# Optimization experiments

Measured on AMD Instinct MI355X. Metric: run time of the kernel, lower is better.

The kernel has to match this reference:

```python
import jax, jax.numpy as jnp
import numpy as np

N = 100000          # nodes
E = 1600000         # directed edges (before self-loops)
F_IN = 500          # num_features
HID = 16            # hidden_dim
HEADS = 8
NUM_CLASSES = 10
NEG_SLOPE = 0.2     # PyG GATConv default
BN_EPS = 1e-5


def setup_inputs() -> dict:
    key = jax.random.key(0)
    ks = jax.random.split(key, 20)
    def glorot(k, shape):
        fan = shape[0] + shape[-1]
        return jax.random.normal(k, shape, jnp.float32) * jnp.sqrt(2.0 / fan)
    x = jax.random.normal(ks[0], (N, F_IN), jnp.float32)
    edge_index = jax.random.randint(ks[1], (2, E), 0, N, dtype=jnp.int32)
    inp = {
        'x': x, 'edge_index': edge_index,
        # conv1: F_IN -> HID, 8 heads
        'W1': glorot(ks[2], (F_IN, HEADS * HID)),
        'a1_src': glorot(ks[3], (HEADS, HID)),
        'a1_dst': glorot(ks[4], (HEADS, HID)),
        'b1': jnp.zeros((HEADS * HID,), jnp.float32),
        'g1': jnp.ones((HEADS * HID,), jnp.float32),
        'be1': jnp.zeros((HEADS * HID,), jnp.float32),
        # conv2: 128 -> HID, 8 heads
        'W2': glorot(ks[5], (HEADS * HID, HEADS * HID)),
        'a2_src': glorot(ks[6], (HEADS, HID)),
        'a2_dst': glorot(ks[7], (HEADS, HID)),
        'b2': jnp.zeros((HEADS * HID,), jnp.float32),
        'g2': jnp.ones((HEADS * HID,), jnp.float32),
        'be2': jnp.zeros((HEADS * HID,), jnp.float32),
        # conv3: 128 -> NUM_CLASSES, 1 head
        'W3': glorot(ks[8], (HEADS * HID, NUM_CLASSES)),
        'a3_src': glorot(ks[9], (1, NUM_CLASSES)),
        'a3_dst': glorot(ks[10], (1, NUM_CLASSES)),
        'b3': jnp.zeros((NUM_CLASSES,), jnp.float32),
    }
    return inp


def gat_conv(x, src, dst, W, a_src, a_dst, b, heads, out_ch):
    n = x.shape[0]
    h = (x @ W).reshape(n, heads, out_ch)                      # [N,H,C]
    al_src = jnp.einsum('nhc,hc->nh', h, a_src)                # [N,H]
    al_dst = jnp.einsum('nhc,hc->nh', h, a_dst)                # [N,H]
    e = al_src[src] + al_dst[dst]                              # [E,H]
    e = jnp.where(e > 0, e, NEG_SLOPE * e)                     # LeakyReLU
    # segment softmax over incoming edges of each dst node
    m = jax.ops.segment_max(e, dst, num_segments=n)            # [N,H]
    m = jnp.where(jnp.isfinite(m), m, 0.0)
    p = jnp.exp(e - m[dst])                                    # [E,H]
    denom = jax.ops.segment_sum(p, dst, num_segments=n)        # [N,H]
    alpha = p / jnp.maximum(denom[dst], 1e-16)                 # [E,H]
    msg = h[src] * alpha[:, :, None]                           # [E,H,C]
    out = jax.ops.segment_sum(msg, dst, num_segments=n)        # [N,H,C]
    return out.reshape(n, heads * out_ch) + b


def batch_norm_eval(x, gamma, beta):
    # eval-mode BN with running_mean=0, running_var=1
    return x * (gamma / jnp.sqrt(1.0 + BN_EPS)) + beta


def reference(x, edge_index, W1, a1_src, a1_dst, b1, g1, be1,
              W2, a2_src, a2_dst, b2, g2, be2,
              W3, a3_src, a3_dst, b3):
    loops = jnp.arange(N, dtype=edge_index.dtype)
    src = jnp.concatenate([edge_index[0], loops])
    dst = jnp.concatenate([edge_index[1], loops])
    h = jax.nn.elu(gat_conv(x, src, dst, W1, a1_src, a1_dst, b1, HEADS, HID))
    h = batch_norm_eval(h, g1, be1)
    h = jax.nn.elu(gat_conv(h, src, dst, W2, a2_src, a2_dst, b2, HEADS, HID))
    h = batch_norm_eval(h, g2, be2)
    h = gat_conv(h, src, dst, W3, a3_src, a3_dst, b3, 1, NUM_CLASSES)
    return jax.nn.log_softmax(h, axis=1)
```

## Files before the change

### kernel.cpp

```cpp
#include <hip/hip_runtime.h>
#include <math.h>

#define N_NODES 100000
#define N_EDGES 1600000
#define ET (N_EDGES + N_NODES)
#define F_IN 500
#define D1 128
#define HEADS 8
#define HID 16
#define NCLS 10
#define MAXDEG 64
#define CSTR 16

using frag = __attribute__((ext_vector_type(8))) short;
using f4   = __attribute__((ext_vector_type(4))) float;

__device__ __forceinline__ unsigned short f2bf(float x) {
    unsigned u = __float_as_uint(x);
    unsigned r = u + 0x7fff + ((u >> 16) & 1);
    return (unsigned short)(r >> 16);
}
__device__ __forceinline__ unsigned short f2bf_tr(float x) {
    return (unsigned short)(__float_as_uint(x) >> 16);
}
__device__ __forceinline__ float bf2f(unsigned short b) {
    return __uint_as_float(((unsigned)b) << 16);
}
__device__ __forceinline__ float bflo(unsigned u) { return __uint_as_float(u << 16); }
__device__ __forceinline__ float bfhi(unsigned u) { return __uint_as_float(u & 0xffff0000u); }
__device__ __forceinline__ float lrelu(float e) { return (e > 0.f) ? e : 0.2f * e; }

__global__ __launch_bounds__(256) void k_scatter(const int* __restrict__ eidx,
                                                 int* __restrict__ cnt,
                                                 int* __restrict__ slots) {
    int base = blockIdx.x * 1024 + threadIdx.x;
#pragma unroll
    for (int k = 0; k < 4; k++) {
        int i = base + k * 256;
        if (i < ET) {
            int s, d;
            if (i < N_EDGES) { s = eidx[i]; d = eidx[N_EDGES + i]; }
            else             { s = i - N_EDGES; d = s; }
            int j = atomicAdd(&cnt[d * CSTR], 1);
            if (j < MAXDEG) slots[d * MAXDEG + j] = s;
        }
    }
}

template<int K, int KP>
__global__ __launch_bounds__(256) void k_pack(const float* __restrict__ W,
                                              short* __restrict__ bhi,
                                              short* __restrict__ blo) {
    int t = blockIdx.x * 256 + threadIdx.x;
    if (t >= KP * 128) return;
    int n = t & 127, k = t >> 7;
    float w = (k < K) ? W[k * 128 + n] : 0.f;
    unsigned short h = f2bf(w);
    unsigned short l = f2bf(w - bf2f(h));
    int kt = k >> 5, kq = (k >> 3) & 3, j = k & 7, nt = n >> 4;
    int lane = kq * 16 + (n & 15);
    int idx = ((kt * 8 + nt) * 64 + lane) * 8 + j;
    bhi[idx] = (short)h;
    blo[idx] = (short)l;
}

template<int K, int NSTEP>
__global__ __launch_bounds__(256, 3) void k_mfma_gemm(const float* __restrict__ A,
                                                      const short* __restrict__ Bhi,
                                                      const short* __restrict__ Blo,
                                                      unsigned* __restrict__ hb, int n) {
    __shared__ short Ah[2][128 * 40];
    __shared__ short Al[2][128 * 40];
    const int tid  = threadIdx.x;
    const int lane = tid & 63;
    const int w    = tid >> 6;
    const int wm   = w >> 1, wn = w & 1;
    const int r0   = blockIdx.x * 128;

    float4 ld[4];
    auto issue_loads = [&](int k0) {
#pragma unroll
        for (int p = 0; p < 4; p++) {
            int c = tid + p * 256;
            int row = r0 + (c >> 3);
            int kk = k0 + ((c & 7) << 2);
            if (row < n && kk < K) ld[p] = *(const float4*)(A + (size_t)row * K + kk);
            else                   ld[p] = float4{0.f, 0.f, 0.f, 0.f};
        }
    };
    auto stage = [&](int buf) {
#pragma unroll
        for (int p = 0; p < 4; p++) {
            int c = tid + p * 256;
            int row = c >> 3;
            int kc = (c & 7) << 2;
            float4 v = ld[p];
            unsigned short h0 = f2bf(v.x), h1 = f2bf(v.y), h2 = f2bf(v.z), h3 = f2bf(v.w);
            unsigned short q0 = f2bf_tr(v.x - bf2f(h0)), q1 = f2bf_tr(v.y - bf2f(h1));
            unsigned short q2 = f2bf_tr(v.z - bf2f(h2)), q3 = f2bf_tr(v.w - bf2f(h3));
            int off = row * 40 + kc;
            *(uint2*)(&Ah[buf][off]) = uint2{(unsigned)h0 | ((unsigned)h1 << 16),
                                             (unsigned)h2 | ((unsigned)h3 << 16)};
            *(uint2*)(&Al[buf][off]) = uint2{(unsigned)q0 | ((unsigned)q1 << 16),
                                             (unsigned)q2 | ((unsigned)q3 << 16)};
        }
    };

    f4 acc[4][4];
#pragma unroll
    for (int a = 0; a < 4; a++)
#pragma unroll
        for (int b = 0; b < 4; b++) acc[a][b] = f4{0.f, 0.f, 0.f, 0.f};

    issue_loads(0);
    int p = 0;
    for (int s = 0; s < NSTEP; s++) {
        stage(p);
        if (s + 1 < NSTEP) issue_loads((s + 1) * 32);
        __syncthreads();
        frag ahi[4], alo[4];
        const int kb = (lane >> 4) * 8;
#pragma unroll
        for (int mt = 0; mt < 4; mt++) {
            int row = wm * 64 + mt * 16 + (lane & 15);
            ahi[mt] = *(const frag*)(&Ah[p][row * 40 + kb]);
            alo[mt] = *(const frag*)(&Al[p][row * 40 + kb]);
        }
#pragma unroll
        for (int nn = 0; nn < 4; nn++) {
            int nt = wn * 4 + nn;
            frag bhi = *(const frag*)(Bhi + (((size_t)s * 8 + nt) * 64 + lane) * 8);
            frag blo = *(const frag*)(Blo + (((size_t)s * 8 + nt) * 64 + lane) * 8);
#pragma unroll
            for (int mt = 0; mt < 4; mt++) {
                acc[mt][nn] = __builtin_amdgcn_mfma_f32_16x16x32_bf16(ahi[mt], bhi, acc[mt][nn], 0, 0, 0);
                acc[mt][nn] = __builtin_amdgcn_mfma_f32_16x16x32_bf16(ahi[mt], blo, acc[mt][nn], 0, 0, 0);
                acc[mt][nn] = __builtin_amdgcn_mfma_f32_16x16x32_bf16(alo[mt], bhi, acc[mt][nn], 0, 0, 0);
            }
        }
        p ^= 1;
    }

#pragma unroll
    for (int mt = 0; mt < 4; mt++) {
        int rowb = r0 + wm * 64 + mt * 16 + (lane >> 4) * 4;
#pragma unroll
        for (int nn = 0; nn < 4; nn++) {
#pragma unroll
            for (int i = 0; i < 4; i++) {
                float v  = acc[mt][nn][i];
                float v2 = __shfl_xor(v, 1);
                int row = rowb + i;
                if (!(lane & 1) && row < n) {
                    unsigned pk = (unsigned)f2bf(v) | ((unsigned)f2bf(v2) << 16);
                    hb[(size_t)row * 64 + wn * 32 + nn * 8 + ((lane & 15) >> 1)] = pk;
                }
            }
        }
    }
}

__global__ __launch_bounds__(256) void k_attn_bf(const unsigned* __restrict__ hb,
                                                 const float* __restrict__ a_src,
                                                 const float* __restrict__ a_dst,
                                                 float* __restrict__ als,
                                                 float* __restrict__ ald, int n) {
    int t = blockIdx.x * blockDim.x + threadIdx.x;
    if (t >= n * 8) return;
    int hd = t & 7;
    const unsigned* hp = hb + (size_t)(t >> 3) * 64 + hd * 8;
    float s1 = 0.f, s2 = 0.f;
#pragma unroll
    for (int j = 0; j < 8; j++) {
        unsigned u = hp[j];
        float v0 = bflo(u), v1 = bfhi(u);
        s1 += v0 * a_src[hd * 16 + 2 * j] + v1 * a_src[hd * 16 + 2 * j + 1];
        s2 += v0 * a_dst[hd * 16 + 2 * j] + v1 * a_dst[hd * 16 + 2 * j + 1];
    }
    als[t] = s1;
    ald[t] = s2;
}

__global__ __launch_bounds__(256) void k_attn3(const float* __restrict__ h,
                                               const float* __restrict__ a_src,
                                               const float* __restrict__ a_dst,
                                               float* __restrict__ als,
                                               float* __restrict__ ald, int n) {
    int t = blockIdx.x * blockDim.x + threadIdx.x;
    if (t >= n) return;
    const float* hp = h + (long)t * NCLS;
    float s1 = 0.f, s2 = 0.f;
#pragma unroll
    for (int cc = 0; cc < NCLS; cc++) {
        float v = hp[cc];
        s1 += v * a_src[cc];
        s2 += v * a_dst[cc];
    }
    als[t] = s1;
    ald[t] = s2;
}

__global__ __launch_bounds__(256) void k_agg128(const unsigned* __restrict__ hb,
                                                const float* __restrict__ als,
                                                const float* __restrict__ ald,
                                                const int* __restrict__ cnt,
                                                const int* __restrict__ slots,
                                                const float* __restrict__ bias,
                                                const float* __restrict__ gamma,
                                                const float* __restrict__ beta,
                                                float* __restrict__ out, int n) {
    int lane = threadIdx.x & 63;
    int node = __builtin_amdgcn_readfirstlane(blockIdx.x * 4 + (threadIdx.x >> 6));
    if (node >= n) return;
    int head = lane >> 3;
    float aldv = ald[node * 8 + head];
    int deg = min(cnt[node * CSTR], MAXDEG);
    const int* sl = slots + (long)node * MAXDEG;

    float l = 0.f, accx = 0.f, accy = 0.f;
    int j = 0;
    for (; j + 1 < deg; j += 2) {
        int s0 = sl[j], s1 = sl[j + 1];
        unsigned u0 = hb[(size_t)s0 * 64 + lane];
        unsigned u1 = hb[(size_t)s1 * 64 + lane];
        float p0 = __expf(lrelu(als[s0 * 8 + head] + aldv));
        float p1 = __expf(lrelu(als[s1 * 8 + head] + aldv));
        l += p0 + p1;
        accx += p0 * bflo(u0) + p1 * bflo(u1);
        accy += p0 * bfhi(u0) + p1 * bfhi(u1);
    }
    if (j < deg) {
        int s0 = sl[j];
        unsigned u0 = hb[(size_t)s0 * 64 + lane];
        float p0 = __expf(lrelu(als[s0 * 8 + head] + aldv));
        l += p0;
        accx += p0 * bflo(u0);
        accy += p0 * bfhi(u0);
    }
    float inv = 1.f / fmaxf(l, 1e-16f);
    const float bnr = rsqrtf(1.0f + 1e-5f);
    int c0 = 2 * lane;
    float v0 = accx * inv + bias[c0];
    v0 = (v0 > 0.f) ? v0 : expm1f(v0);
    v0 = v0 * (gamma[c0] * bnr) + beta[c0];
    float v1 = accy * inv + bias[c0 + 1];
    v1 = (v1 > 0.f) ? v1 : expm1f(v1);
    v1 = v1 * (gamma[c0 + 1] * bnr) + beta[c0 + 1];
    out[(long)node * 128 + c0]     = v0;
    out[(long)node * 128 + c0 + 1] = v1;
}

__global__ __launch_bounds__(256) void k_gemm_w3(const float* __restrict__ A,
                                                 const float* __restrict__ W,
                                                 float* __restrict__ out, int n) {
    __shared__ float w[D1 * NCLS];
    for (int idx = threadIdx.x; idx < D1 * NCLS; idx += 256) w[idx] = W[idx];
    __syncthreads();
    int node = blockIdx.x * 256 + threadIdx.x;
    if (node >= n) return;
    const float* ar = A + (long)node * D1;
    float acc[NCLS];
#pragma unroll
    for (int cc = 0; cc < NCLS; cc++) acc[cc] = 0.f;
    for (int k = 0; k < D1; k++) {
        float av = ar[k];
#pragma unroll
        for (int cc = 0; cc < NCLS; cc++) acc[cc] = fmaf(av, w[k * NCLS + cc], acc[cc]);
    }
#pragma unroll
    for (int cc = 0; cc < NCLS; cc++) out[(long)node * NCLS + cc] = acc[cc];
}

__global__ __launch_bounds__(256) void k_agg3(const float* __restrict__ h3,
                                              const float* __restrict__ als,
                                              const float* __restrict__ ald,
                                              const int* __restrict__ cnt,
                                              const int* __restrict__ slots,
                                              const float* __restrict__ b3,
                                              float* __restrict__ out, int n) {
    int lane = threadIdx.x & 63;
    int node = __builtin_amdgcn_readfirstlane(blockIdx.x * 4 + (threadIdx.x >> 6));
    if (node >= n) return;
    int g = lane >> 4, r = lane & 15;
    float aldv = ald[node];
    int deg = min(cnt[node * CSTR], MAXDEG);
    const int* sl = slots + (long)node * MAXDEG;

    float l = 0.f, acc = 0.f;
    for (int j = g; j < deg; j += 4) {
        int s = sl[j];
        float p = __expf(lrelu(als[s] + aldv));
        l += p;
        acc += p * ((r < NCLS) ? h3[(long)s * NCLS + r] : 0.f);
    }
    l   += __shfl_xor(l, 16);   l   += __shfl_xor(l, 32);
    acc += __shfl_xor(acc, 16); acc += __shfl_xor(acc, 32);

    float z = acc / fmaxf(l, 1e-16f) + ((r < NCLS) ? b3[r] : 0.f);
    float zm = (r < NCLS) ? z : -INFINITY;
#pragma unroll
    for (int off = 8; off > 0; off >>= 1) zm = fmaxf(zm, __shfl_xor(zm, off));
    float pe = (r < NCLS) ? __expf(z - zm) : 0.f;
#pragma unroll
    for (int off = 8; off > 0; off >>= 1) pe += __shfl_xor(pe, off);
    if (g == 0 && r < NCLS) out[(long)node * NCLS + r] = z - zm - logf(pe);
}

extern "C" void kernel_launch(void* const* d_in, const int* in_sizes, int n_in,
                              void* d_out, int out_size, void* d_ws, size_t ws_size,
                              hipStream_t stream) {
    const float* x   = (const float*)d_in[0];
    const int*   eix = (const int*)  d_in[1];
    const float* W1  = (const float*)d_in[2];
    const float* a1s = (const float*)d_in[3];
    const float* a1d = (const float*)d_in[4];
    const float* b1  = (const float*)d_in[5];
    const float* g1  = (const float*)d_in[6];
    const float* be1 = (const float*)d_in[7];
    const float* W2  = (const float*)d_in[8];
    const float* a2s = (const float*)d_in[9];
    const float* a2d = (const float*)d_in[10];
    const float* b2  = (const float*)d_in[11];
    const float* g2  = (const float*)d_in[12];
    const float* be2 = (const float*)d_in[13];
    const float* W3  = (const float*)d_in[14];
    const float* a3s = (const float*)d_in[15];
    const float* a3d = (const float*)d_in[16];
    const float* b3  = (const float*)d_in[17];
    float* out = (float*)d_out;

    unsigned* hb  = (unsigned*)d_ws;
    float* feat   = (float*)(hb + (size_t)N_NODES * 64);
    float* h3     = feat + (size_t)N_NODES * 128;
    float* als    = h3   + (size_t)N_NODES * 16;
    float* ald    = als  + (size_t)N_NODES * HEADS;
    int*   cnt    = (int*)(ald + (size_t)N_NODES * HEADS);
    int*   slots  = cnt + (size_t)N_NODES * CSTR;
    short* b1hi   = (short*)(slots + (size_t)N_NODES * MAXDEG);
    short* b1lo   = b1hi + 512 * 128;
    short* b2hi   = b1lo + 512 * 128;
    short* b2lo   = b2hi + 128 * 128;

    hipMemsetAsync(cnt, 0, (size_t)N_NODES * CSTR * sizeof(int), stream);
    k_scatter<<<(ET + 1023) / 1024, 256, 0, stream>>>(eix, cnt, slots);
    k_pack<F_IN, 512><<<(512 * 128 + 255) / 256, 256, 0, stream>>>(W1, b1hi, b1lo);
    k_pack<D1, 128><<<(128 * 128 + 255) / 256, 256, 0, stream>>>(W2, b2hi, b2lo);

    const int gemm_grid = (N_NODES + 127) / 128;

    k_mfma_gemm<F_IN, 16><<<gemm_grid, 256, 0, stream>>>(x, b1hi, b1lo, hb, N_NODES);
    k_attn_bf<<<(N_NODES * 8 + 255) / 256, 256, 0, stream>>>(hb, a1s, a1d, als, ald, N_NODES);
    k_agg128<<<(N_NODES + 3) / 4, 256, 0, stream>>>(hb, als, ald, cnt, slots, b1, g1, be1, feat, N_NODES);

    k_mfma_gemm<D1, 4><<<gemm_grid, 256, 0, stream>>>(feat, b2hi, b2lo, hb, N_NODES);
    k_attn_bf<<<(N_NODES * 8 + 255) / 256, 256, 0, stream>>>(hb, a2s, a2d, als, ald, N_NODES);
    k_agg128<<<(N_NODES + 3) / 4, 256, 0, stream>>>(hb, als, ald, cnt, slots, b2, g2, be2, feat, N_NODES);

    k_gemm_w3<<<(N_NODES + 255) / 256, 256, 0, stream>>>(feat, W3, h3, N_NODES);
    k_attn3<<<(N_NODES + 255) / 256, 256, 0, stream>>>(h3, a3s, a3d, als, ald, N_NODES);
    k_agg3<<<(N_NODES + 3) / 4, 256, 0, stream>>>(h3, als, ald, cnt, slots, b3, out, N_NODES);
}
```

Before: 766.8 us.

## Build CSR adjacency via per-XCC destination binning and LDS bucket assembly

Replaces the direct global-atomic scatter of edges into per-node slot lists with a two-pass build. The first pass appends packed (src, local dst) pairs into coarse bins keyed by 256-node destination block and XCC id. The second pass assembles each block's slot lists with shared-memory atomics and writes them out with coalesced int4 stores. This removes the large padded counter memset and the random global atomics and slot writes, but adds contention on far fewer bin counters, an extra pass over the edges, 64KB of LDS per block, and fixed bin capacities that silently drop edges if exceeded.

```diff
diff --git a/kernel.cpp b/kernel.cpp
--- a/kernel.cpp
+++ b/kernel.cpp
@@ -10,7 +10,10 @@
 #define HID 16
 #define NCLS 10
 #define MAXDEG 64
-#define CSTR 16
+#define NB 391
+#define NSUB 8
+#define CAPS 1024
+#define CPAD 16
 
 using frag = __attribute__((ext_vector_type(8))) short;
 using f4   = __attribute__((ext_vector_type(4))) float;
@@ -30,9 +33,11 @@
 __device__ __forceinline__ float bfhi(unsigned u) { return __uint_as_float(u & 0xffff0000u); }
 __device__ __forceinline__ float lrelu(float e) { return (e > 0.f) ? e : 0.2f * e; }
 
-__global__ __launch_bounds__(256) void k_scatter(const int* __restrict__ eidx,
-                                                 int* __restrict__ cnt,
-                                                 int* __restrict__ slots) {
+__global__ __launch_bounds__(256) void k_bin(const int* __restrict__ eidx,
+                                             int* __restrict__ bincnt,
+                                             int* __restrict__ bin) {
+    unsigned xcc;
+    asm("s_getreg_b32 %0, hwreg(HW_REG_XCC_ID)" : "=s"(xcc));
     int base = blockIdx.x * 1024 + threadIdx.x;
 #pragma unroll
     for (int k = 0; k < 4; k++) {
@@ -41,10 +46,42 @@
             int s, d;
             if (i < N_EDGES) { s = eidx[i]; d = eidx[N_EDGES + i]; }
             else             { s = i - N_EDGES; d = s; }
-            int j = atomicAdd(&cnt[d * CSTR], 1);
-            if (j < MAXDEG) slots[d * MAXDEG + j] = s;
-        }
-    }
+            int sb = (d >> 8) * NSUB + (int)xcc;
+            int pos = atomicAdd(&bincnt[sb * CPAD], 1);
+            if (pos < CAPS) bin[(size_t)sb * CAPS + pos] = (s << 8) | (d & 255);
+        }
+    }
+}
+
+__global__ __launch_bounds__(256) void k_build(const int* __restrict__ bincnt,
+                                               const int* __restrict__ bin,
+                                               int* __restrict__ cnt,
+                                               int* __restrict__ slots) {
+    __shared__ int lcnt[256];
+    __shared__ int lsl[256 * MAXDEG];
+    const int b   = blockIdx.x;
+    const int tid = threadIdx.x;
+    lcnt[tid] = 0;
+    __syncthreads();
+    for (int sub = 0; sub < NSUB; sub++) {
+        int sb = b * NSUB + sub;
+        int len = min(bincnt[sb * CPAD], CAPS);
+        const int* bp = bin + (size_t)sb * CAPS;
+        for (int i = tid; i < len; i += 256) {
+            int v = bp[i];
+            int doff = v & 255;
+            int j = atomicAdd(&lcnt[doff], 1);
+            if (j < MAXDEG) lsl[doff * MAXDEG + j] = v >> 8;
+        }
+    }
+    __syncthreads();
+    int node0 = b * 256;
+    int nloc = min(256, N_NODES - node0);
+    if (tid < nloc) cnt[node0 + tid] = min(lcnt[tid], MAXDEG);
+    int total4 = (nloc * MAXDEG) >> 2;
+    int4* dst4 = (int4*)(slots + (size_t)node0 * MAXDEG);
+    const int4* src4 = (const int4*)lsl;
+    for (int i = tid; i < total4; i += 256) dst4[i] = src4[i];
 }
 
 template<int K, int KP>
@@ -214,7 +251,7 @@
     if (node >= n) return;
     int head = lane >> 3;
     float aldv = ald[node * 8 + head];
-    int deg = min(cnt[node * CSTR], MAXDEG);
+    int deg = min(cnt[node], MAXDEG);
     const int* sl = slots + (long)node * MAXDEG;
 
     float l = 0.f, accx = 0.f, accy = 0.f;
@@ -283,7 +320,7 @@
     if (node >= n) return;
     int g = lane >> 4, r = lane & 15;
     float aldv = ald[node];
-    int deg = min(cnt[node * CSTR], MAXDEG);
+    int deg = min(cnt[node], MAXDEG);
     const int* sl = slots + (long)node * MAXDEG;
 
     float l = 0.f, acc = 0.f;
@@ -335,14 +372,18 @@
     float* als    = h3   + (size_t)N_NODES * 16;
     float* ald    = als  + (size_t)N_NODES * HEADS;
     int*   cnt    = (int*)(ald + (size_t)N_NODES * HEADS);
-    int*   slots  = cnt + (size_t)N_NODES * CSTR;
+    int*   slots  = cnt + (size_t)N_NODES;
     short* b1hi   = (short*)(slots + (size_t)N_NODES * MAXDEG);
     short* b1lo   = b1hi + 512 * 128;
     short* b2hi   = b1lo + 512 * 128;
     short* b2lo   = b2hi + 128 * 128;
 
-    hipMemsetAsync(cnt, 0, (size_t)N_NODES * CSTR * sizeof(int), stream);
-    k_scatter<<<(ET + 1023) / 1024, 256, 0, stream>>>(eix, cnt, slots);
+    int* bincnt = (int*)feat;
+    int* bin    = bincnt + (size_t)NB * NSUB * CPAD;
+
+    hipMemsetAsync(bincnt, 0, (size_t)NB * NSUB * CPAD * sizeof(int), stream);
+    k_bin<<<(ET + 1023) / 1024, 256, 0, stream>>>(eix, bincnt, bin);
+    k_build<<<NB, 256, 0, stream>>>(bincnt, bin, cnt, slots);
     k_pack<F_IN, 512><<<(512 * 128 + 255) / 256, 256, 0, stream>>>(W1, b1hi, b1lo);
     k_pack<D1, 128><<<(128 * 128 + 255) / 256, 256, 0, stream>>>(W2, b2hi, b2lo);
 
```

After: 779.3 us. About the same (+1.6%).
